# Performance work log

Hardware: AMD Instinct MI355X
Metric: run time of the kernel (lower is better)

## Reference

```python
import jax, jax.numpy as jnp
import numpy as np

L, BS, D, H, R = 2048, 16, 512, 8, 48
DH = D // H          # 64 head dim
HID = 4 * D          # 2048 mlp hidden
BN_EPS = 1e-5


def _bn(x, g, b, m, v):
    # inference-mode BatchNorm1d over last dim
    return (x - m) * (g * jax.lax.rsqrt(v + BN_EPS)) + b


def _mem(x, w_tau):
    # MembraneIntegrator: m_t = beta*m_{t-1} + (1-beta)*x_t, scan over L
    tau = jax.nn.softplus(w_tau) + 1.0
    beta = jnp.clip(1.0 - 1.0 / tau, 0.0, 0.9999)  # [D]
    def step(m, xt):
        m = beta * m + (1.0 - beta) * xt
        return m, m
    m0 = jnp.zeros(x.shape[1:], x.dtype)
    _, out = jax.lax.scan(step, m0, x)
    return out  # [L,BS,D]


def _split(t):
    # [L,BS,D] -> [BS,H,L,DH]
    Lx, Bx, _ = t.shape
    return t.reshape(Lx, Bx, H, DH).transpose(1, 2, 0, 3)


def _rff(x, W, b):
    # nonneg random-feature map: elu(xW+b)+1+1e-6, scaled by 1/sqrt(R)
    proj = jnp.einsum('bhld,hdr->bhlr', x, W) + b[None, :, None, :]
    phi = jax.nn.elu(proj) + (1.0 + 1e-6)
    return phi * np.float32(1.0 / np.sqrt(R))


def setup_inputs() -> dict:
    key = jax.random.key(0)
    ks = iter(jax.random.split(key, 64))
    def nrm(shape, s=1.0):
        return jax.random.normal(next(ks), shape, jnp.float32) * np.float32(s)
    def uni(shape):
        return jax.random.uniform(next(ks), shape, jnp.float32)
    inp = {'x': nrm((L, BS, D))}
    for name, dim in [('bn1', D), ('bnq', D), ('bnk', D), ('bnv', D),
                      ('bn2', D), ('bnf1', HID), ('bnf2', D)]:
        inp[name + '_g'] = uni((dim,)) + 0.5
        inp[name + '_b'] = nrm((dim,), 0.1)
        inp[name + '_m'] = nrm((dim,), 0.1)
        inp[name + '_v'] = uni((dim,)) + 0.5
    s = 1.0 / np.sqrt(D)
    inp['Wq'] = nrm((D, D), s); inp['Wk'] = nrm((D, D), s)
    inp['Wv'] = nrm((D, D), s); inp['bv'] = nrm((D,), 0.02)
    inp['Wo'] = nrm((D, D), s); inp['bo'] = nrm((D,), 0.02)
    inp['wtau_q'] = nrm((D,), 0.1)
    inp['wtau_k'] = nrm((D,), 0.1)
    inp['rff_W'] = nrm((H, DH, R), 1.0 / np.sqrt(DH))
    inp['rff_b'] = uni((H, R)) * np.float32(2 * np.pi)
    inp['fc1_W'] = nrm((D, HID), s); inp['fc1_b'] = nrm((HID,), 0.02)
    inp['fc2_W'] = nrm((HID, D), 1.0 / np.sqrt(HID)); inp['fc2_b'] = nrm((D,), 0.02)
    return inp


def reference(x, bn1_g, bn1_b, bn1_m, bn1_v, Wq, Wk, Wv, bv, Wo, bo,
              bnq_g, bnq_b, bnq_m, bnq_v, bnk_g, bnk_b, bnk_m, bnk_v,
              bnv_g, bnv_b, bnv_m, bnv_v, wtau_q, wtau_k, rff_W, rff_b,
              bn2_g, bn2_b, bn2_m, bn2_v, fc1_W, fc1_b,
              bnf1_g, bnf1_b, bnf1_m, bnf1_v, fc2_W, fc2_b,
              bnf2_g, bnf2_b, bnf2_m, bnf2_v):
    # --- attention branch ---
    h1 = _bn(x, bn1_g, bn1_b, bn1_m, bn1_v)
    q_in = _bn(h1 @ Wq, bnq_g, bnq_b, bnq_m, bnq_v)
    k_in = _bn(h1 @ Wk, bnk_g, bnk_b, bnk_m, bnk_v)
    v_in = _bn(h1 @ Wv + bv, bnv_g, bnv_b, bnv_m, bnv_v)
    Q = _mem(q_in, wtau_q)
    K = _mem(k_in, wtau_k)
    q = _split(Q); k = _split(K); v = _split(v_in)   # [BS,H,L,DH]
    phi_q = _rff(q, rff_W, rff_b)                    # [BS,H,L,R]
    phi_k = _rff(k, rff_W, rff_b)
    K_sum = jnp.clip(phi_k.sum(axis=2), 1e-6, None)  # [BS,H,R]
    KV = jnp.einsum('bhlr,bhld->bhrd', phi_k, v)     # [BS,H,R,DH]
    num = jnp.einsum('bhlr,bhrd->bhld', phi_q, KV)
    den = jnp.einsum('bhlr,bhr->bhl', phi_q, K_sum)[..., None] + 1e-6
    attn = (num / den).transpose(2, 0, 1, 3).reshape(L, BS, D)
    x = x + (attn @ Wo + bo)
    # --- ffn branch ---
    h2 = _bn(x, bn2_g, bn2_b, bn2_m, bn2_v)
    f = _bn(h2 @ fc1_W + fc1_b, bnf1_g, bnf1_b, bnf1_m, bnf1_v)
    f = jax.nn.gelu(f, approximate=False)
    f = _bn(f @ fc2_W + fc2_b, bnf2_g, bnf2_b, bnf2_m, bnf2_v)
    return x + f
```

## Files before the change

### kernel.cpp

```cpp
#include <hip/hip_runtime.h>
#include <hip/hip_bf16.h>
#include <cstdint>
#include <math.h>


typedef float  f32x4 __attribute__((ext_vector_type(4)));
typedef short  s16x8 __attribute__((ext_vector_type(8)));
typedef unsigned short u16x4 __attribute__((ext_vector_type(4)));

#define DEV static __device__ __forceinline__

constexpr int NR = 32768;

DEV float us2f(unsigned short u) {
  union { unsigned int i; float f; } z; z.i = ((unsigned int)u) << 16; return z.f;
}
DEV unsigned short f2bits(float f) {
  unsigned int u = __builtin_bit_cast(unsigned int, f);
  unsigned int r = u + 0x7fffu + ((u >> 16) & 1u);
  return (unsigned short)(r >> 16);
}

DEV void gload_lds16(const void* g, void* l) {
  __builtin_amdgcn_global_load_lds((__attribute__((address_space(1))) void*)g,
                                   (__attribute__((address_space(3))) void*)l, 16, 0, 0);
}

struct PrepArgs {
  const float *g[7], *b[7], *m[7], *v[7];
  const float *wtq, *wtk;
  float *s[7], *t[7];
  float *betaq, *betak;
  float *dotqkv, *dot1;
};

__global__ void prep_vectors(PrepArgs a) {
  int i = blockIdx.x * 256 + threadIdx.x;
  const int dims[7] = {512, 512, 512, 512, 512, 2048, 512};
  #pragma unroll
  for (int k = 0; k < 7; ++k) {
    if (i < dims[k]) {
      float sc = a.g[k][i] * rsqrtf(a.v[k][i] + 1e-5f);
      a.s[k][i] = sc;
      a.t[k][i] = a.b[k][i] - a.m[k][i] * sc;
    }
  }
  if (i < 1536) a.dotqkv[i] = 0.f;
  if (i < 2048) a.dot1[i] = 0.f;
  if (i < 512) {
    float w = a.wtq[i];
    float sp = (w > 20.f) ? w : log1pf(expf(w));
    float be = 1.f - 1.f / (sp + 1.f);
    a.betaq[i] = fminf(fmaxf(be, 0.f), 0.9999f);
    w = a.wtk[i];
    sp = (w > 20.f) ? w : log1pf(expf(w));
    be = 1.f - 1.f / (sp + 1.f);
    a.betak[i] = fminf(fmaxf(be, 0.f), 0.9999f);
  }
}

__global__ void fold_wT2(const float* __restrict__ W, int K, int Nn,
                         const float* scin, const float* scout,
                         const float* tin, float* dotacc,
                         unsigned short* __restrict__ WT) {
  __shared__ float tile[64][65];
  __shared__ float dsum[4][64];
  const int j0 = blockIdx.x * 64, d0 = blockIdx.y * 64;
  const int tid = threadIdx.x;
  const int j = tid & 63, r = tid >> 6;
  float dpart = 0.f;
  #pragma unroll
  for (int i = 0; i < 16; ++i) {
    int dd = i * 4 + r;
    float w = W[(size_t)(d0 + dd) * Nn + j0 + j];
    tile[dd][j] = w;
    if (tin) dpart += tin[d0 + dd] * w;
  }
  if (tin) dsum[r][j] = dpart;
  __syncthreads();
  if (tin && r == 0)
    atomicAdd(&dotacc[j0 + j], dsum[0][j] + dsum[1][j] + dsum[2][j] + dsum[3][j]);
  const int d = j;
  const float si = scin ? scin[d0 + d] : 1.f;
  #pragma unroll
  for (int i = 0; i < 16; ++i) {
    int jj = i * 4 + r;
    float so = scout ? scout[j0 + jj] : 1.f;
    WT[(size_t)(j0 + jj) * K + d0 + d] = f2bits(tile[d][jj] * si * so);
  }
}

__global__ void fold_wT(const float* __restrict__ W, int K, int Nn,
                        unsigned short* __restrict__ WT) {
  int j = blockIdx.x;
  int lane = threadIdx.x;
  for (int dd = lane; dd < K; dd += 64)
    WT[(size_t)j * K + dd] = f2bits(W[(size_t)dd * Nn + j]);
}

struct BiasArgs {
  const float *dotqkv, *dot1, *bv, *fc1b, *fc2b;
  const float *s1, *t1, *s2, *t2, *s3, *t3, *s5, *t5, *s6, *t6;
  float *c_qkv, *c1, *c2;
};
__global__ void bias_fin(BiasArgs a) {
  int i = blockIdx.x * 256 + threadIdx.x;
  if (i < 512) {
    a.c_qkv[i]        = a.s1[i] * a.dotqkv[i]        + a.t1[i];
    a.c_qkv[512 + i]  = a.s2[i] * a.dotqkv[512 + i]  + a.t2[i];
    a.c_qkv[1024 + i] = a.s3[i] * (a.dotqkv[1024 + i] + a.bv[i]) + a.t3[i];
    a.c2[i]           = a.s6[i] * a.fc2b[i] + a.t6[i];
  }
  if (i < 2048) a.c1[i] = a.s5[i] * (a.dot1[i] + a.fc1b[i]) + a.t5[i];
}

__global__ void cast_x(const float* __restrict__ x, unsigned short* __restrict__ xb, int n) {
  int i = (blockIdx.x * blockDim.x + threadIdx.x) * 4;
  if (i >= n) return;
  float4 v = *(const float4*)(x + i);
  u16x4 o = {f2bits(v.x), f2bits(v.y), f2bits(v.z), f2bits(v.w)};
  *(u16x4*)(xb + i) = o;
}

template <int MODE>
__global__ __launch_bounds__(256, 4) void gemm_bf16(
    const unsigned short* __restrict__ A, const unsigned short* __restrict__ BT,
    int K, int Nn, const float* __restrict__ bias,
    const unsigned short* __restrict__ xresb,
    float* __restrict__ outf, unsigned short* __restrict__ outb) {
  __shared__ __align__(16) unsigned short Ab[2][128 * 32];
  __shared__ __align__(16) unsigned short Bb[2][128 * 32];
  const int tid = threadIdx.x, w = tid >> 6, lane = tid & 63;
  const int l15 = lane & 15, lg = lane >> 4;
  const int row0 = blockIdx.x * 128, col0 = blockIdx.y * 128;
  const int wr = w >> 1, wc = w & 1;
  const unsigned short* Abase = A + (size_t)row0 * K;
  const unsigned short* Bbase = BT + (size_t)col0 * K;

  auto stage = [&](int buf, int kt) {
    #pragma unroll
    for (int s = 0; s < 2; ++s) {
      int c = s * 256 + w * 64 + lane;
      gload_lds16(Abase + (size_t)(c >> 2) * K + kt * 32 + (c & 3) * 8,
                  &Ab[buf][(s * 256 + w * 64) * 8]);
      gload_lds16(Bbase + (size_t)(c >> 2) * K + kt * 32 + (c & 3) * 8,
                  &Bb[buf][(s * 256 + w * 64) * 8]);
    }
  };

  const f32x4 fz = {0.f, 0.f, 0.f, 0.f};
  f32x4 acc[4][4];
  #pragma unroll
  for (int m = 0; m < 4; ++m)
    #pragma unroll
    for (int n = 0; n < 4; ++n) acc[m][n] = fz;

  stage(0, 0);
  __syncthreads();
  int cur = 0;
  const int nt = K >> 5;
  for (int kt = 0; kt < nt; ++kt) {
    if (kt + 1 < nt) stage(cur ^ 1, kt + 1);
    s16x8 af[4], bf[4];
    #pragma unroll
    for (int m = 0; m < 4; ++m)
      af[m] = *(const s16x8*)&Ab[cur][(wr * 64 + m * 16 + l15) * 32 + lg * 8];
    #pragma unroll
    for (int n = 0; n < 4; ++n)
      bf[n] = *(const s16x8*)&Bb[cur][(wc * 64 + n * 16 + l15) * 32 + lg * 8];
    #pragma unroll
    for (int m = 0; m < 4; ++m)
      #pragma unroll
      for (int n = 0; n < 4; ++n)
        acc[m][n] = __builtin_amdgcn_mfma_f32_16x16x32_bf16(af[m], bf[n], acc[m][n], 0, 0, 0);
    __syncthreads();
    cur ^= 1;
  }

  #pragma unroll
  for (int m = 0; m < 4; ++m) {
    #pragma unroll
    for (int q = 0; q < 4; ++q) {
      int row = row0 + wr * 64 + m * 16 + lg * 4 + q;
      #pragma unroll
      for (int n = 0; n < 4; ++n) {
        int col = col0 + wc * 64 + n * 16 + l15;
        float v = acc[m][n][q] + bias[col];
        size_t idx = (size_t)row * Nn + col;
        if constexpr (MODE == 0) {
          outb[idx] = f2bits(v);
        } else if constexpr (MODE == 1) {
          outb[idx] = f2bits(us2f(xresb[idx]) + v);
        } else if constexpr (MODE == 2) {
          float u2 = v * 1.5957691216f * (1.f + 0.044715f * v * v);
          float gl = v / (1.f + __expf(-u2));
          outb[idx] = f2bits(gl);
        } else {
          outf[idx] = us2f(xresb[idx]) + v;
        }
      }
    }
  }
}

__global__ __launch_bounds__(1024) void mem_scan2(unsigned short* __restrict__ qkv,
                         const float* __restrict__ betaq, const float* __restrict__ betak) {
  __shared__ float carry[16][64];
  __shared__ float pre[16][64];
  int cg = blockIdx.x & 15, b = blockIdx.x >> 4;
  int w = threadIdx.x >> 6, lane = threadIdx.x & 63;
  int ch = cg * 64 + lane;
  const float beta = (ch < 512) ? betaq[ch] : betak[ch - 512];
  const float om = 1.f - beta;
  unsigned short* base = qkv + (size_t)b * 1536 + ch;
  const size_t rs = 16 * 1536;
  const int l0 = w * 128;

  float m = 0.f;
  for (int i = 0; i < 128; i += 8) {
    float v[8];
    #pragma unroll
    for (int j = 0; j < 8; ++j) v[j] = us2f(base[(size_t)(l0 + i + j) * rs]);
    #pragma unroll
    for (int j = 0; j < 8; ++j) m = beta * m + om * v[j];
  }
  carry[w][lane] = m;
  __syncthreads();
  if (w == 0) {
    float pw = beta;
    #pragma unroll
    for (int t = 0; t < 7; ++t) pw *= pw;
    float run = 0.f;
    for (int cc = 0; cc < 16; ++cc) {
      pre[cc][lane] = run;
      run = carry[cc][lane] + pw * run;
    }
  }
  __syncthreads();
  m = pre[w][lane];
  for (int i = 0; i < 128; i += 8) {
    float v[8];
    #pragma unroll
    for (int j = 0; j < 8; ++j) v[j] = us2f(base[(size_t)(l0 + i + j) * rs]);
    #pragma unroll
    for (int j = 0; j < 8; ++j) {
      m = beta * m + om * v[j];
      base[(size_t)(l0 + i + j) * rs] = f2bits(m);
    }
  }
}

__global__ void transpose_v(const unsigned short* __restrict__ qkv, unsigned short* __restrict__ vT) {
  __shared__ __align__(16) unsigned short tile[64][72];
  int bid = blockIdx.x;
  int lt = bid & 31, h = (bid >> 5) & 7, b = bid >> 8;
  int l0 = lt * 64;
  int tid = threadIdx.x;
  int r = tid >> 2, cg = (tid & 3) * 16;
  const unsigned short* src = qkv + (size_t)((l0 + r) * 16 + b) * 1536 + 1024 + h * 64 + cg;
  *(s16x8*)&tile[r][cg] = *(const s16x8*)(src);
  *(s16x8*)&tile[r][cg + 8] = *(const s16x8*)(src + 8);
  __syncthreads();
  int dh = tid >> 2, lgp = (tid & 3) * 16;
  s16x8 o0, o1;
  #pragma unroll
  for (int j = 0; j < 8; ++j) {
    o0[j] = (short)tile[lgp + j][dh];
    o1[j] = (short)tile[lgp + 8 + j][dh];
  }
  unsigned short* dstp = vT + (size_t)((b * 8 + h) * 64 + dh) * 2048 + l0 + lgp;
  *(s16x8*)dstp = o0;
  *(s16x8*)(dstp + 8) = o1;
}

__global__ __launch_bounds__(512, 1) void attn_A(
    const unsigned short* __restrict__ qkv, const unsigned short* __restrict__ vT,
    const unsigned short* __restrict__ WrT, const float* __restrict__ rffb,
    float* __restrict__ KVg, float* __restrict__ Ksumg) {
  __shared__ float KV[48][64];
  __shared__ float Ksum[48];
  __shared__ __align__(16) unsigned short phiT[8][48][72];

  const int tid = threadIdx.x;
  const int w = tid >> 6, lane = tid & 63, l15 = lane & 15, lg = lane >> 4;
  const int bh = blockIdx.x, b = bh >> 3, h = bh & 7;
  const int half = blockIdx.y;
  const f32x4 fz = {0.f, 0.f, 0.f, 0.f};
  constexpr float ISR = 0.14433756729740643f;

  for (int i = tid; i < 48 * 64; i += 512) (&KV[0][0])[i] = 0.f;
  if (tid < 48) Ksum[tid] = 0.f;
  __syncthreads();

  s16x8 wf[3][2];
  float bias_n[3];
  #pragma unroll
  for (int n = 0; n < 3; ++n) {
    int r = n * 16 + l15;
    bias_n[n] = rffb[h * 48 + r];
    #pragma unroll
    for (int ks = 0; ks < 2; ++ks)
      wf[n][ks] = *(const s16x8*)(WrT + (size_t)(h * 48 + r) * 64 + ks * 32 + lg * 8);
  }

  f32x4 kv[3][4];
  #pragma unroll
  for (int mm = 0; mm < 3; ++mm)
    #pragma unroll
    for (int nn = 0; nn < 4; ++nn) kv[mm][nn] = fz;
  float ks_acc[3] = {0.f, 0.f, 0.f};
  const size_t vbase = (size_t)(b * 8 + h) * 64 * 2048;

  for (int c = half * 16 + w; c < half * 16 + 16; c += 8) {
    const int l0 = c * 64;
    s16x8 kf[4][2];
    #pragma unroll
    for (int m = 0; m < 4; ++m) {
      size_t ro = (size_t)((l0 + m * 16 + l15) * 16 + b) * 1536 + 512 + h * 64;
      #pragma unroll
      for (int ks = 0; ks < 2; ++ks)
        kf[m][ks] = *(const s16x8*)(qkv + ro + ks * 32 + lg * 8);
    }
    f32x4 p[4][3];
    #pragma unroll
    for (int m = 0; m < 4; ++m)
      #pragma unroll
      for (int n = 0; n < 3; ++n) {
        p[m][n] = fz + bias_n[n];
        #pragma unroll
        for (int ks = 0; ks < 2; ++ks)
          p[m][n] = __builtin_amdgcn_mfma_f32_16x16x32_bf16(kf[m][ks], wf[n][ks], p[m][n], 0, 0, 0);
      }
    #pragma unroll
    for (int m = 0; m < 4; ++m)
      #pragma unroll
      for (int n = 0; n < 3; ++n) {
        u16x4 pk;
        #pragma unroll
        for (int q = 0; q < 4; ++q) {
          float pv = p[m][n][q];
          float ph = (pv > 0.f ? pv + 1.000001f : __expf(pv) + 1e-6f) * ISR;
          ks_acc[n] += ph;
          pk[q] = f2bits(ph);
        }
        *(u16x4*)&phiT[w][n * 16 + l15][m * 16 + lg * 4] = pk;
      }
    s16x8 pf[3][2], vf[4][2];
    #pragma unroll
    for (int mm = 0; mm < 3; ++mm)
      #pragma unroll
      for (int ks = 0; ks < 2; ++ks)
        pf[mm][ks] = *(const s16x8*)&phiT[w][mm * 16 + l15][ks * 32 + lg * 8];
    #pragma unroll
    for (int nn = 0; nn < 4; ++nn)
      #pragma unroll
      for (int ks = 0; ks < 2; ++ks)
        vf[nn][ks] = *(const s16x8*)(vT + vbase + (size_t)(nn * 16 + l15) * 2048 + l0 + ks * 32 + lg * 8);
    #pragma unroll
    for (int mm = 0; mm < 3; ++mm)
      #pragma unroll
      for (int nn = 0; nn < 4; ++nn)
        #pragma unroll
        for (int ks = 0; ks < 2; ++ks)
          kv[mm][nn] = __builtin_amdgcn_mfma_f32_16x16x32_bf16(pf[mm][ks], vf[nn][ks], kv[mm][nn], 0, 0, 0);
  }
  #pragma unroll
  for (int n = 0; n < 3; ++n) {
    float t = ks_acc[n];
    t += __shfl_xor(t, 16);
    t += __shfl_xor(t, 32);
    if (lane < 16) atomicAdd(&Ksum[n * 16 + lane], t);
  }
  #pragma unroll
  for (int mm = 0; mm < 3; ++mm)
    #pragma unroll
    for (int nn = 0; nn < 4; ++nn)
      #pragma unroll
      for (int q = 0; q < 4; ++q)
        atomicAdd(&KV[mm * 16 + lg * 4 + q][nn * 16 + l15], kv[mm][nn][q]);
  __syncthreads();

  float* dst = KVg + (size_t)(half * 128 + bh) * 3072;
  for (int i = tid; i < 48 * 64; i += 512) dst[i] = (&KV[0][0])[i];
  if (tid < 48) Ksumg[(half * 128 + bh) * 48 + tid] = Ksum[tid];
}

__global__ __launch_bounds__(512, 1) void attn_B(
    const unsigned short* __restrict__ qkv, const unsigned short* __restrict__ WrT,
    const float* __restrict__ rffb, const float* __restrict__ KVg,
    const float* __restrict__ Ksumg, unsigned short* __restrict__ attn) {
  __shared__ __align__(16) unsigned short KVT[80][72];
  __shared__ __align__(16) unsigned short phiQ[8][64][72];

  const int tid = threadIdx.x;
  const int w = tid >> 6, lane = tid & 63, l15 = lane & 15, lg = lane >> 4;
  const int bh = blockIdx.x, b = bh >> 3, h = bh & 7;
  const int half = blockIdx.y;
  const f32x4 fz = {0.f, 0.f, 0.f, 0.f};
  constexpr float ISR = 0.14433756729740643f;

  for (int i = tid; i < 8 * 64 * 72; i += 512) (&phiQ[0][0][0])[i] = 0;
  for (int i = tid; i < 80 * 72; i += 512) {
    int dhe = i / 72, rr = i - dhe * 72;
    float val = 0.f;
    if (rr < 48) {
      if (dhe < 64)
        val = KVg[(size_t)bh * 3072 + rr * 64 + dhe] + KVg[(size_t)(128 + bh) * 3072 + rr * 64 + dhe];
      else if (dhe == 64)
        val = fmaxf(Ksumg[bh * 48 + rr] + Ksumg[(128 + bh) * 48 + rr], 1e-6f);
    }
    (&KVT[0][0])[i] = f2bits(val);
  }
  __syncthreads();

  s16x8 wf[3][2];
  float bias_n[3];
  #pragma unroll
  for (int n = 0; n < 3; ++n) {
    int r = n * 16 + l15;
    bias_n[n] = rffb[h * 48 + r];
    #pragma unroll
    for (int ks = 0; ks < 2; ++ks)
      wf[n][ks] = *(const s16x8*)(WrT + (size_t)(h * 48 + r) * 64 + ks * 32 + lg * 8);
  }

  for (int c = half * 16 + w; c < half * 16 + 16; c += 8) {
    const int l0 = c * 64;
    s16x8 qf[4][2];
    #pragma unroll
    for (int m = 0; m < 4; ++m) {
      size_t ro = (size_t)((l0 + m * 16 + l15) * 16 + b) * 1536 + h * 64;
      #pragma unroll
      for (int ks = 0; ks < 2; ++ks)
        qf[m][ks] = *(const s16x8*)(qkv + ro + ks * 32 + lg * 8);
    }
    f32x4 p[4][3];
    #pragma unroll
    for (int m = 0; m < 4; ++m)
      #pragma unroll
      for (int n = 0; n < 3; ++n) {
        p[m][n] = fz + bias_n[n];
        #pragma unroll
        for (int ks = 0; ks < 2; ++ks)
          p[m][n] = __builtin_amdgcn_mfma_f32_16x16x32_bf16(qf[m][ks], wf[n][ks], p[m][n], 0, 0, 0);
      }
    #pragma unroll
    for (int m = 0; m < 4; ++m)
      #pragma unroll
      for (int n = 0; n < 3; ++n)
        #pragma unroll
        for (int q = 0; q < 4; ++q) {
          float pv = p[m][n][q];
          float ph = (pv > 0.f ? pv + 1.000001f : __expf(pv) + 1e-6f) * ISR;
          phiQ[w][m * 16 + lg * 4 + q][n * 16 + l15] = f2bits(ph);
        }
    s16x8 af[4][2], bv8[5][2];
    #pragma unroll
    for (int m = 0; m < 4; ++m)
      #pragma unroll
      for (int ks = 0; ks < 2; ++ks)
        af[m][ks] = *(const s16x8*)&phiQ[w][m * 16 + l15][ks * 32 + lg * 8];
    #pragma unroll
    for (int n5 = 0; n5 < 5; ++n5)
      #pragma unroll
      for (int ks = 0; ks < 2; ++ks)
        bv8[n5][ks] = *(const s16x8*)&KVT[n5 * 16 + l15][ks * 32 + lg * 8];
    f32x4 o[4][5];
    #pragma unroll
    for (int m = 0; m < 4; ++m)
      #pragma unroll
      for (int n5 = 0; n5 < 5; ++n5) {
        o[m][n5] = fz;
        #pragma unroll
        for (int ks = 0; ks < 2; ++ks)
          o[m][n5] = __builtin_amdgcn_mfma_f32_16x16x32_bf16(af[m][ks], bv8[n5][ks], o[m][n5], 0, 0, 0);
      }
    #pragma unroll
    for (int m = 0; m < 4; ++m)
      #pragma unroll
      for (int q = 0; q < 4; ++q) {
        float den = __shfl(o[m][4][q], lane & 48);
        float inv = 1.f / (den + 1e-6f);
        int gl = l0 + m * 16 + lg * 4 + q;
        size_t ob = (size_t)(gl * 16 + b) * 512 + h * 64;
        #pragma unroll
        for (int n = 0; n < 4; ++n)
          attn[ob + n * 16 + l15] = f2bits(o[m][n][q] * inv);
      }
  }
}

extern "C" void kernel_launch(void* const* d_in, const int* in_sizes, int n_in,
                              void* d_out, int out_size, void* d_ws, size_t ws_size,
                              hipStream_t stream) {
  (void)in_sizes; (void)n_in; (void)out_size; (void)ws_size;
  const float* x = (const float*)d_in[0];
  const float* Wq = (const float*)d_in[29];
  const float* Wk = (const float*)d_in[30];
  const float* Wv = (const float*)d_in[31];
  const float* bv = (const float*)d_in[32];
  const float* Wo = (const float*)d_in[33];
  const float* bo = (const float*)d_in[34];
  const float* wtq = (const float*)d_in[35];
  const float* wtk = (const float*)d_in[36];
  const float* rffW = (const float*)d_in[37];
  const float* rffb = (const float*)d_in[38];
  const float* fc1W = (const float*)d_in[39];
  const float* fc1b = (const float*)d_in[40];
  const float* fc2W = (const float*)d_in[41];
  const float* fc2b = (const float*)d_in[42];

  char* cur = (char*)d_ws;
  auto alloc = [&](size_t bytes) -> char* {
    char* r = cur;
    cur += (bytes + 255) & ~(size_t)255;
    return r;
  };
  float* sv_[7];
  float* tv_[7];
  const int dims[7] = {512, 512, 512, 512, 512, 2048, 512};
  for (int k = 0; k < 7; ++k) {
    sv_[k] = (float*)alloc(dims[k] * 4);
    tv_[k] = (float*)alloc(dims[k] * 4);
  }
  float* betaq = (float*)alloc(512 * 4);
  float* betak = (float*)alloc(512 * 4);
  float* c_qkv = (float*)alloc(1536 * 4);
  float* c1 = (float*)alloc(2048 * 4);
  float* c2 = (float*)alloc(512 * 4);
  float* dotqkv = (float*)alloc(1536 * 4);
  float* dot1   = (float*)alloc(2048 * 4);
  float* KVg   = (float*)alloc((size_t)256 * 3072 * 4);
  float* Ksumg = (float*)alloc((size_t)256 * 48 * 4);
  unsigned short* AqkvT = (unsigned short*)alloc((size_t)1536 * 512 * 2);
  unsigned short* WoT   = (unsigned short*)alloc((size_t)512 * 512 * 2);
  unsigned short* A1T   = (unsigned short*)alloc((size_t)2048 * 512 * 2);
  unsigned short* A2T   = (unsigned short*)alloc((size_t)512 * 2048 * 2);
  unsigned short* WrT   = (unsigned short*)alloc((size_t)8 * 48 * 64 * 2);
  unsigned short* qkv   = (unsigned short*)alloc((size_t)NR * 1536 * 2);
  unsigned short* vT    = (unsigned short*)alloc((size_t)NR * 512 * 2);
  unsigned short* xb    = (unsigned short*)alloc((size_t)NR * 512 * 2);
  unsigned short* xrb   = (unsigned short*)alloc((size_t)NR * 512 * 2);
  unsigned short* attnO = vT;
  unsigned short* g = qkv;

  PrepArgs pa;
  for (int k = 0; k < 7; ++k) {
    pa.g[k] = (const float*)d_in[1 + k * 4 + 0];
    pa.b[k] = (const float*)d_in[1 + k * 4 + 1];
    pa.m[k] = (const float*)d_in[1 + k * 4 + 2];
    pa.v[k] = (const float*)d_in[1 + k * 4 + 3];
    pa.s[k] = sv_[k];
    pa.t[k] = tv_[k];
  }
  pa.wtq = wtq; pa.wtk = wtk; pa.betaq = betaq; pa.betak = betak;
  pa.dotqkv = dotqkv; pa.dot1 = dot1;

  prep_vectors<<<8, 256, 0, stream>>>(pa);
  fold_wT2<<<dim3(8, 8), 256, 0, stream>>>(Wq, 512, 512, sv_[0], sv_[1], tv_[0], dotqkv, AqkvT);
  fold_wT2<<<dim3(8, 8), 256, 0, stream>>>(Wk, 512, 512, sv_[0], sv_[2], tv_[0], dotqkv + 512, AqkvT + 512 * 512);
  fold_wT2<<<dim3(8, 8), 256, 0, stream>>>(Wv, 512, 512, sv_[0], sv_[3], tv_[0], dotqkv + 1024, AqkvT + 1024 * 512);
  fold_wT2<<<dim3(8, 8), 256, 0, stream>>>(Wo, 512, 512, nullptr, nullptr, nullptr, nullptr, WoT);
  fold_wT2<<<dim3(32, 8), 256, 0, stream>>>(fc1W, 512, 2048, sv_[4], sv_[5], tv_[4], dot1, A1T);
  fold_wT2<<<dim3(8, 32), 256, 0, stream>>>(fc2W, 2048, 512, nullptr, sv_[6], nullptr, nullptr, A2T);
  for (int h = 0; h < 8; ++h)
    fold_wT<<<48, 64, 0, stream>>>(rffW + h * 64 * 48, 64, 48, WrT + h * 48 * 64);

  BiasArgs ba;
  ba.dotqkv = dotqkv; ba.dot1 = dot1; ba.bv = bv; ba.fc1b = fc1b; ba.fc2b = fc2b;
  ba.s1 = sv_[1]; ba.t1 = tv_[1]; ba.s2 = sv_[2]; ba.t2 = tv_[2]; ba.s3 = sv_[3]; ba.t3 = tv_[3];
  ba.s5 = sv_[5]; ba.t5 = tv_[5]; ba.s6 = sv_[6]; ba.t6 = tv_[6];
  ba.c_qkv = c_qkv; ba.c1 = c1; ba.c2 = c2;
  bias_fin<<<8, 256, 0, stream>>>(ba);

  cast_x<<<16384, 256, 0, stream>>>(x, xb, NR * 512);
  gemm_bf16<0><<<dim3(256, 12), 256, 0, stream>>>(xb, AqkvT, 512, 1536, c_qkv, nullptr, nullptr, qkv);
  mem_scan2<<<256, 1024, 0, stream>>>(qkv, betaq, betak);
  transpose_v<<<4096, 256, 0, stream>>>(qkv, vT);
  attn_A<<<dim3(128, 2), 512, 0, stream>>>(qkv, vT, WrT, rffb, KVg, Ksumg);
  attn_B<<<dim3(128, 2), 512, 0, stream>>>(qkv, WrT, rffb, KVg, Ksumg, attnO);
  gemm_bf16<1><<<dim3(256, 4), 256, 0, stream>>>(attnO, WoT, 512, 512, bo, xb, nullptr, xrb);
  gemm_bf16<2><<<dim3(256, 16), 256, 0, stream>>>(xrb, A1T, 512, 2048, c1, nullptr, nullptr, g);
  gemm_bf16<3><<<dim3(256, 4), 256, 0, stream>>>(g, A2T, 2048, 512, c2, xrb, (float*)d_out, nullptr);
}
```

Baseline: 545.4 us.

## Split attention kernels into four L-chunks per head and cut register and LDS use

Both linear-attention kernels now launch four blocks per batch-head instead of two, so each wave handles a single 64-row chunk instead of looping over two. attn_A accumulates KV per mm/nn tile straight into LDS atomics instead of keeping a 48-register accumulator array. attn_B processes one 16-row sub-tile at a time, which shrinks its phiQ LDS buffer, and launch bounds rise to allow four blocks per CU. The aim is more occupancy and parallelism in these small kernels. In exchange there are more LDS atomics, and attn_B must reduce four partial KV/Ksum buffers instead of two.

```diff
diff --git a/kernel.cpp b/kernel.cpp
--- a/kernel.cpp
+++ b/kernel.cpp
@@ -273,7 +273,7 @@
   *(s16x8*)(dstp + 8) = o1;
 }
 
-__global__ __launch_bounds__(512, 1) void attn_A(
+__global__ __launch_bounds__(512, 4) void attn_A(
     const unsigned short* __restrict__ qkv, const unsigned short* __restrict__ vT,
     const unsigned short* __restrict__ WrT, const float* __restrict__ rffb,
     float* __restrict__ KVg, float* __restrict__ Ksumg) {
@@ -284,7 +284,7 @@
   const int tid = threadIdx.x;
   const int w = tid >> 6, lane = tid & 63, l15 = lane & 15, lg = lane >> 4;
   const int bh = blockIdx.x, b = bh >> 3, h = bh & 7;
-  const int half = blockIdx.y;
+  const int l0 = (blockIdx.y * 8 + w) * 64;
   const f32x4 fz = {0.f, 0.f, 0.f, 0.f};
   constexpr float ISR = 0.14433756729740643f;
 
@@ -303,67 +303,34 @@
       wf[n][ks] = *(const s16x8*)(WrT + (size_t)(h * 48 + r) * 64 + ks * 32 + lg * 8);
   }
 
-  f32x4 kv[3][4];
-  #pragma unroll
-  for (int mm = 0; mm < 3; ++mm)
-    #pragma unroll
-    for (int nn = 0; nn < 4; ++nn) kv[mm][nn] = fz;
+  f32x4 p[4][3];
+  #pragma unroll
+  for (int m = 0; m < 4; ++m) {
+    size_t ro = (size_t)((l0 + m * 16 + l15) * 16 + b) * 1536 + 512 + h * 64;
+    s16x8 kf0 = *(const s16x8*)(qkv + ro + lg * 8);
+    s16x8 kf1 = *(const s16x8*)(qkv + ro + 32 + lg * 8);
+    #pragma unroll
+    for (int n = 0; n < 3; ++n) {
+      p[m][n] = fz + bias_n[n];
+      p[m][n] = __builtin_amdgcn_mfma_f32_16x16x32_bf16(kf0, wf[n][0], p[m][n], 0, 0, 0);
+      p[m][n] = __builtin_amdgcn_mfma_f32_16x16x32_bf16(kf1, wf[n][1], p[m][n], 0, 0, 0);
+    }
+  }
   float ks_acc[3] = {0.f, 0.f, 0.f};
-  const size_t vbase = (size_t)(b * 8 + h) * 64 * 2048;
-
-  for (int c = half * 16 + w; c < half * 16 + 16; c += 8) {
-    const int l0 = c * 64;
-    s16x8 kf[4][2];
-    #pragma unroll
-    for (int m = 0; m < 4; ++m) {
-      size_t ro = (size_t)((l0 + m * 16 + l15) * 16 + b) * 1536 + 512 + h * 64;
+  #pragma unroll
+  for (int m = 0; m < 4; ++m)
+    #pragma unroll
+    for (int n = 0; n < 3; ++n) {
+      u16x4 pk;
       #pragma unroll
-      for (int ks = 0; ks < 2; ++ks)
-        kf[m][ks] = *(const s16x8*)(qkv + ro + ks * 32 + lg * 8);
-    }
-    f32x4 p[4][3];
-    #pragma unroll
-    for (int m = 0; m < 4; ++m)
-      #pragma unroll
-      for (int n = 0; n < 3; ++n) {
-        p[m][n] = fz + bias_n[n];
-        #pragma unroll
-        for (int ks = 0; ks < 2; ++ks)
-          p[m][n] = __builtin_amdgcn_mfma_f32_16x16x32_bf16(kf[m][ks], wf[n][ks], p[m][n], 0, 0, 0);
+      for (int q = 0; q < 4; ++q) {
+        float pv = p[m][n][q];
+        float ph = (pv > 0.f ? pv + 1.000001f : __expf(pv) + 1e-6f) * ISR;
+        ks_acc[n] += ph;
+        pk[q] = f2bits(ph);
       }
-    #pragma unroll
-    for (int m = 0; m < 4; ++m)
-      #pragma unroll
-      for (int n = 0; n < 3; ++n) {
-        u16x4 pk;
-        #pragma unroll
-        for (int q = 0; q < 4; ++q) {
-          float pv = p[m][n][q];
-          float ph = (pv > 0.f ? pv + 1.000001f : __expf(pv) + 1e-6f) * ISR;
-          ks_acc[n] += ph;
-          pk[q] = f2bits(ph);
-        }
-        *(u16x4*)&phiT[w][n * 16 + l15][m * 16 + lg * 4] = pk;
-      }
-    s16x8 pf[3][2], vf[4][2];
-    #pragma unroll
-    for (int mm = 0; mm < 3; ++mm)
-      #pragma unroll
-      for (int ks = 0; ks < 2; ++ks)
-        pf[mm][ks] = *(const s16x8*)&phiT[w][mm * 16 + l15][ks * 32 + lg * 8];
-    #pragma unroll
-    for (int nn = 0; nn < 4; ++nn)
-      #pragma unroll
-      for (int ks = 0; ks < 2; ++ks)
-        vf[nn][ks] = *(const s16x8*)(vT + vbase + (size_t)(nn * 16 + l15) * 2048 + l0 + ks * 32 + lg * 8);
-    #pragma unroll
-    for (int mm = 0; mm < 3; ++mm)
-      #pragma unroll
-      for (int nn = 0; nn < 4; ++nn)
-        #pragma unroll
-        for (int ks = 0; ks < 2; ++ks)
-          kv[mm][nn] = __builtin_amdgcn_mfma_f32_16x16x32_bf16(pf[mm][ks], vf[nn][ks], kv[mm][nn], 0, 0, 0);
-  }
+      *(u16x4*)&phiT[w][n * 16 + l15][m * 16 + lg * 4] = pk;
+    }
   #pragma unroll
   for (int n = 0; n < 3; ++n) {
     float t = ks_acc[n];
@@ -371,43 +338,63 @@
     t += __shfl_xor(t, 32);
     if (lane < 16) atomicAdd(&Ksum[n * 16 + lane], t);
   }
-  #pragma unroll
-  for (int mm = 0; mm < 3; ++mm)
-    #pragma unroll
-    for (int nn = 0; nn < 4; ++nn)
+
+  const size_t vbase = (size_t)(b * 8 + h) * 64 * 2048;
+  #pragma unroll
+  for (int nn = 0; nn < 4; ++nn) {
+    size_t vo = vbase + (size_t)(nn * 16 + l15) * 2048 + l0;
+    s16x8 vf0 = *(const s16x8*)(vT + vo + lg * 8);
+    s16x8 vf1 = *(const s16x8*)(vT + vo + 32 + lg * 8);
+    #pragma unroll
+    for (int mm = 0; mm < 3; ++mm) {
+      s16x8 pf0 = *(const s16x8*)&phiT[w][mm * 16 + l15][lg * 8];
+      s16x8 pf1 = *(const s16x8*)&phiT[w][mm * 16 + l15][32 + lg * 8];
+      f32x4 a = fz;
+      a = __builtin_amdgcn_mfma_f32_16x16x32_bf16(pf0, vf0, a, 0, 0, 0);
+      a = __builtin_amdgcn_mfma_f32_16x16x32_bf16(pf1, vf1, a, 0, 0, 0);
       #pragma unroll
       for (int q = 0; q < 4; ++q)
-        atomicAdd(&KV[mm * 16 + lg * 4 + q][nn * 16 + l15], kv[mm][nn][q]);
-  __syncthreads();
-
-  float* dst = KVg + (size_t)(half * 128 + bh) * 3072;
+        atomicAdd(&KV[mm * 16 + lg * 4 + q][nn * 16 + l15], a[q]);
+    }
+  }
+  __syncthreads();
+
+  float* dst = KVg + (size_t)(blockIdx.y * 128 + bh) * 3072;
   for (int i = tid; i < 48 * 64; i += 512) dst[i] = (&KV[0][0])[i];
-  if (tid < 48) Ksumg[(half * 128 + bh) * 48 + tid] = Ksum[tid];
-}
-
-__global__ __launch_bounds__(512, 1) void attn_B(
+  if (tid < 48) Ksumg[(blockIdx.y * 128 + bh) * 48 + tid] = Ksum[tid];
+}
+
+__global__ __launch_bounds__(512, 4) void attn_B(
     const unsigned short* __restrict__ qkv, const unsigned short* __restrict__ WrT,
     const float* __restrict__ rffb, const float* __restrict__ KVg,
     const float* __restrict__ Ksumg, unsigned short* __restrict__ attn) {
   __shared__ __align__(16) unsigned short KVT[80][72];
-  __shared__ __align__(16) unsigned short phiQ[8][64][72];
+  __shared__ __align__(16) unsigned short phiQ[8][16][72];
 
   const int tid = threadIdx.x;
   const int w = tid >> 6, lane = tid & 63, l15 = lane & 15, lg = lane >> 4;
   const int bh = blockIdx.x, b = bh >> 3, h = bh & 7;
-  const int half = blockIdx.y;
+  const int l0 = (blockIdx.y * 8 + w) * 64;
   const f32x4 fz = {0.f, 0.f, 0.f, 0.f};
   constexpr float ISR = 0.14433756729740643f;
 
-  for (int i = tid; i < 8 * 64 * 72; i += 512) (&phiQ[0][0][0])[i] = 0;
+  for (int i = lane; i < 16 * 24; i += 64) {
+    int rr = i / 24, cc = 48 + i - (i / 24) * 24;
+    phiQ[w][rr][cc] = 0;
+  }
   for (int i = tid; i < 80 * 72; i += 512) {
     int dhe = i / 72, rr = i - dhe * 72;
     float val = 0.f;
     if (rr < 48) {
-      if (dhe < 64)
-        val = KVg[(size_t)bh * 3072 + rr * 64 + dhe] + KVg[(size_t)(128 + bh) * 3072 + rr * 64 + dhe];
-      else if (dhe == 64)
-        val = fmaxf(Ksumg[bh * 48 + rr] + Ksumg[(128 + bh) * 48 + rr], 1e-6f);
+      if (dhe < 64) {
+        val = KVg[(size_t)bh * 3072 + rr * 64 + dhe]
+            + KVg[(size_t)(128 + bh) * 3072 + rr * 64 + dhe]
+            + KVg[(size_t)(256 + bh) * 3072 + rr * 64 + dhe]
+            + KVg[(size_t)(384 + bh) * 3072 + rr * 64 + dhe];
+      } else if (dhe == 64) {
+        val = fmaxf(Ksumg[bh * 48 + rr] + Ksumg[(128 + bh) * 48 + rr]
+                  + Ksumg[(256 + bh) * 48 + rr] + Ksumg[(384 + bh) * 48 + rr], 1e-6f);
+      }
     }
     (&KVT[0][0])[i] = f2bits(val);
   }
@@ -424,69 +411,47 @@
       wf[n][ks] = *(const s16x8*)(WrT + (size_t)(h * 48 + r) * 64 + ks * 32 + lg * 8);
   }
 
-  for (int c = half * 16 + w; c < half * 16 + 16; c += 8) {
-    const int l0 = c * 64;
-    s16x8 qf[4][2];
-    #pragma unroll
-    for (int m = 0; m < 4; ++m) {
-      size_t ro = (size_t)((l0 + m * 16 + l15) * 16 + b) * 1536 + h * 64;
-      #pragma unroll
-      for (int ks = 0; ks < 2; ++ks)
-        qf[m][ks] = *(const s16x8*)(qkv + ro + ks * 32 + lg * 8);
-    }
-    f32x4 p[4][3];
-    #pragma unroll
-    for (int m = 0; m < 4; ++m)
-      #pragma unroll
-      for (int n = 0; n < 3; ++n) {
-        p[m][n] = fz + bias_n[n];
-        #pragma unroll
-        for (int ks = 0; ks < 2; ++ks)
-          p[m][n] = __builtin_amdgcn_mfma_f32_16x16x32_bf16(qf[m][ks], wf[n][ks], p[m][n], 0, 0, 0);
-      }
-    #pragma unroll
-    for (int m = 0; m < 4; ++m)
-      #pragma unroll
-      for (int n = 0; n < 3; ++n)
-        #pragma unroll
-        for (int q = 0; q < 4; ++q) {
-          float pv = p[m][n][q];
-          float ph = (pv > 0.f ? pv + 1.000001f : __expf(pv) + 1e-6f) * ISR;
-          phiQ[w][m * 16 + lg * 4 + q][n * 16 + l15] = f2bits(ph);
-        }
-    s16x8 af[4][2], bv8[5][2];
-    #pragma unroll
-    for (int m = 0; m < 4; ++m)
-      #pragma unroll
-      for (int ks = 0; ks < 2; ++ks)
-        af[m][ks] = *(const s16x8*)&phiQ[w][m * 16 + l15][ks * 32 + lg * 8];
-    #pragma unroll
-    for (int n5 = 0; n5 < 5; ++n5)
-      #pragma unroll
-      for (int ks = 0; ks < 2; ++ks)
-        bv8[n5][ks] = *(const s16x8*)&KVT[n5 * 16 + l15][ks * 32 + lg * 8];
-    f32x4 o[4][5];
-    #pragma unroll
-    for (int m = 0; m < 4; ++m)
-      #pragma unroll
-      for (int n5 = 0; n5 < 5; ++n5) {
-        o[m][n5] = fz;
-        #pragma unroll
-        for (int ks = 0; ks < 2; ++ks)
-          o[m][n5] = __builtin_amdgcn_mfma_f32_16x16x32_bf16(af[m][ks], bv8[n5][ks], o[m][n5], 0, 0, 0);
-      }
-    #pragma unroll
-    for (int m = 0; m < 4; ++m)
+  #pragma unroll
+  for (int m = 0; m < 4; ++m) {
+    size_t ro = (size_t)((l0 + m * 16 + l15) * 16 + b) * 1536 + h * 64;
+    s16x8 qf0 = *(const s16x8*)(qkv + ro + lg * 8);
+    s16x8 qf1 = *(const s16x8*)(qkv + ro + 32 + lg * 8);
+    f32x4 pm[3];
+    #pragma unroll
+    for (int n = 0; n < 3; ++n) {
+      pm[n] = fz + bias_n[n];
+      pm[n] = __builtin_amdgcn_mfma_f32_16x16x32_bf16(qf0, wf[n][0], pm[n], 0, 0, 0);
+      pm[n] = __builtin_amdgcn_mfma_f32_16x16x32_bf16(qf1, wf[n][1], pm[n], 0, 0, 0);
+    }
+    #pragma unroll
+    for (int n = 0; n < 3; ++n)
       #pragma unroll
       for (int q = 0; q < 4; ++q) {
-        float den = __shfl(o[m][4][q], lane & 48);
-        float inv = 1.f / (den + 1e-6f);
-        int gl = l0 + m * 16 + lg * 4 + q;
-        size_t ob = (size_t)(gl * 16 + b) * 512 + h * 64;
-        #pragma unroll
-        for (int n = 0; n < 4; ++n)
-          attn[ob + n * 16 + l15] = f2bits(o[m][n][q] * inv);
+        float pv = pm[n][q];
+        float ph = (pv > 0.f ? pv + 1.000001f : __expf(pv) + 1e-6f) * ISR;
+        phiQ[w][lg * 4 + q][n * 16 + l15] = f2bits(ph);
       }
+    s16x8 af0 = *(const s16x8*)&phiQ[w][l15][lg * 8];
+    s16x8 af1 = *(const s16x8*)&phiQ[w][l15][32 + lg * 8];
+    f32x4 o[5];
+    #pragma unroll
+    for (int n5 = 0; n5 < 5; ++n5) {
+      s16x8 b0 = *(const s16x8*)&KVT[n5 * 16 + l15][lg * 8];
+      s16x8 b1 = *(const s16x8*)&KVT[n5 * 16 + l15][32 + lg * 8];
+      o[n5] = fz;
+      o[n5] = __builtin_amdgcn_mfma_f32_16x16x32_bf16(af0, b0, o[n5], 0, 0, 0);
+      o[n5] = __builtin_amdgcn_mfma_f32_16x16x32_bf16(af1, b1, o[n5], 0, 0, 0);
+    }
+    #pragma unroll
+    for (int q = 0; q < 4; ++q) {
+      float den = __shfl(o[4][q], lane & 48);
+      float inv = 1.f / (den + 1e-6f);
+      int gl = l0 + m * 16 + lg * 4 + q;
+      size_t ob = (size_t)(gl * 16 + b) * 512 + h * 64;
+      #pragma unroll
+      for (int n = 0; n < 4; ++n)
+        attn[ob + n * 16 + l15] = f2bits(o[n][q] * inv);
+    }
   }
 }
 
@@ -530,8 +495,8 @@
   float* c2 = (float*)alloc(512 * 4);
   float* dotqkv = (float*)alloc(1536 * 4);
   float* dot1   = (float*)alloc(2048 * 4);
-  float* KVg   = (float*)alloc((size_t)256 * 3072 * 4);
-  float* Ksumg = (float*)alloc((size_t)256 * 48 * 4);
+  float* KVg   = (float*)alloc((size_t)512 * 3072 * 4);
+  float* Ksumg = (float*)alloc((size_t)512 * 48 * 4);
   unsigned short* AqkvT = (unsigned short*)alloc((size_t)1536 * 512 * 2);
   unsigned short* WoT   = (unsigned short*)alloc((size_t)512 * 512 * 2);
   unsigned short* A1T   = (unsigned short*)alloc((size_t)2048 * 512 * 2);
@@ -577,8 +542,8 @@
   gemm_bf16<0><<<dim3(256, 12), 256, 0, stream>>>(xb, AqkvT, 512, 1536, c_qkv, nullptr, nullptr, qkv);
   mem_scan2<<<256, 1024, 0, stream>>>(qkv, betaq, betak);
   transpose_v<<<4096, 256, 0, stream>>>(qkv, vT);
-  attn_A<<<dim3(128, 2), 512, 0, stream>>>(qkv, vT, WrT, rffb, KVg, Ksumg);
-  attn_B<<<dim3(128, 2), 512, 0, stream>>>(qkv, WrT, rffb, KVg, Ksumg, attnO);
+  attn_A<<<dim3(128, 4), 512, 0, stream>>>(qkv, vT, WrT, rffb, KVg, Ksumg);
+  attn_B<<<dim3(128, 4), 512, 0, stream>>>(qkv, WrT, rffb, KVg, Ksumg, attnO);
   gemm_bf16<1><<<dim3(256, 4), 256, 0, stream>>>(attnO, WoT, 512, 512, bo, xb, nullptr, xrb);
   gemm_bf16<2><<<dim3(256, 16), 256, 0, stream>>>(xrb, A1T, 512, 2048, c1, nullptr, nullptr, g);
   gemm_bf16<3><<<dim3(256, 4), 256, 0, stream>>>(g, A2T, 2048, 512, c2, xrb, (float*)d_out, nullptr);
```

Result: slower. 582.1 us (+6.7%).
